# Performance work log

Hardware: AMD Instinct MI355X
Metric: run time of the kernel (lower is better)

Reference implementation:

```python
import jax, jax.numpy as jnp
import numpy as np

N = 500_000   # num nodes
F = 128       # num_features
H = 128       # hidden
B = 32_768    # batch size
K = 4         # hops
RWS = 16      # random walks per batch node
E = RWS * B   # sampled edges per hop
ALPHA = 0.1
OUT = 8


def setup_inputs() -> dict:
    key = jax.random.key(0)
    ks = jax.random.split(key, 12)
    x = jax.random.normal(ks[0], (N, F), dtype=jnp.float32)
    degree = jax.random.uniform(ks[1], (N,), dtype=jnp.float32, minval=1.0, maxval=64.0)
    batch = jax.random.randint(ks[2], (B,), 0, N, dtype=jnp.int32)
    heads_idx = jax.random.randint(ks[3], (K, E), 0, B, dtype=jnp.int32)
    ends = jax.random.randint(ks[4], (K, E), 0, N, dtype=jnp.int32)
    # MLP params (Kaiming-ish scaling)
    W0 = jax.random.normal(ks[5], (F, H), dtype=jnp.float32) / np.float32(np.sqrt(F))
    b0 = jnp.zeros((H,), dtype=jnp.float32)
    W1 = jax.random.normal(ks[6], (H, H), dtype=jnp.float32) / np.float32(np.sqrt(H))
    b1 = jnp.zeros((H,), dtype=jnp.float32)
    W2 = jax.random.normal(ks[7], (H, OUT), dtype=jnp.float32) / np.float32(np.sqrt(H))
    b2 = jnp.zeros((OUT,), dtype=jnp.float32)
    # APPNP attention weights: alpha*(1-alpha)^k, last = (1-alpha)^K
    att = np.float32(ALPHA) * np.float32(1.0 - ALPHA) ** np.arange(K + 1, dtype=np.float32)
    att[-1] = np.float32(1.0 - ALPHA) ** np.float32(K)
    att = jnp.asarray(att)
    return {"x": x, "W0": W0, "b0": b0, "W1": W1, "b1": b1, "W2": W2, "b2": b2,
            "att": att, "degree": degree, "batch": batch,
            "heads_idx": heads_idx, "ends": ends}


def reference(x, W0, b0, W1, b1, W2, b2, att, degree, batch, heads_idx, ends):
    # eval mode: dropout is a no-op
    dis = degree ** -0.5  # deg_inv_sqrt

    def mlp(feats):  # lins[1](relu(lins[0](feats)))
        h = jax.nn.relu(feats @ W0 + b0)
        return h @ W1 + b1

    nb = batch.shape[0]
    ne = jnp.float32(ends.shape[1])
    dsum = degree[batch].sum()

    aggx = att[0] * mlp(x[batch])                       # [B, H]
    for k in range(K):  # small fixed hop count
        heads = heads_idx[k]                            # local rows in [0, B)
        e = ends[k]                                     # global node ids
        val = dis[batch[heads]] * dis[e] * (dsum / ne)  # [E]
        tmp = mlp(x[e]) * val[:, None]                  # gather + MLP + weight
        aggx = aggx + att[k + 1] * jax.ops.segment_sum(tmp, heads, num_segments=nb)
    out = jax.nn.relu(aggx) @ W2 + b2                   # [B, 8]
    return jax.nn.log_softmax(out, axis=1)
```

## Files before the change

kernel.cpp:

```cpp
#include <hip/hip_runtime.h>

#define NN 500000
#define FF 128
#define HH 128
#define BB 32768
#define KHOPS 4
#define EPER 524288
#define KE (KHOPS * EPER)
#define NOUT 8
#define SBLK 512
#define EPB (KE / SBLK)

typedef unsigned short u16;
typedef unsigned char u8;
typedef __attribute__((ext_vector_type(8))) short short8v;
typedef __attribute__((ext_vector_type(4))) float f32x4;

__device__ __forceinline__ float bflo(unsigned int u) {
    union { unsigned int x; float f; } t; t.x = u << 16; return t.f;
}
__device__ __forceinline__ float bfhi(unsigned int u) {
    union { unsigned int x; float f; } t; t.x = u & 0xFFFF0000u; return t.f;
}
__device__ __forceinline__ u16 f2bf(float f) {
    union { float f; unsigned int u; } t; t.f = f;
    unsigned int u = t.u;
    unsigned int r = (u + 0x7FFFu + ((u >> 16) & 1u)) >> 16;
    return (u16)r;
}

__global__ void k_degsum1(const float* __restrict__ deg, const int* __restrict__ batch,
                          float* __restrict__ partial) {
    __shared__ float red[256];
    int i = blockIdx.x * 256 + threadIdx.x;
    red[threadIdx.x] = deg[batch[i]];
    __syncthreads();
    for (int off = 128; off > 0; off >>= 1) {
        if (threadIdx.x < off) red[threadIdx.x] += red[threadIdx.x + off];
        __syncthreads();
    }
    if (threadIdx.x == 0) partial[blockIdx.x] = red[0];
}
__global__ void k_degsum2(const float* __restrict__ partial, float* __restrict__ dsum) {
    __shared__ float red[128];
    red[threadIdx.x] = partial[threadIdx.x];
    __syncthreads();
    for (int off = 64; off > 0; off >>= 1) {
        if (threadIdx.x < off) red[threadIdx.x] += red[threadIdx.x + off];
        __syncthreads();
    }
    if (threadIdx.x == 0) *dsum = red[0];
}

__global__ void k_prep(const float* __restrict__ deg, const int* __restrict__ batch,
                       const float* __restrict__ dsum,
                       float* __restrict__ dis, float* __restrict__ disb) {
    int i = blockIdx.x * 256 + threadIdx.x;
    if (i < NN) dis[i] = rsqrtf(deg[i]);
    if (i < BB) disb[i] = rsqrtf(deg[batch[i]]) * (dsum[0] * (1.0f / (float)EPER));
}

__launch_bounds__(256, 2)
__global__ void k_hist2(const int* __restrict__ heads, u8* __restrict__ M) {
    __shared__ unsigned int hp[8192];
    int tid = threadIdx.x, blk = blockIdx.x;
    #pragma unroll
    for (int j = 0; j < 32; j++) hp[tid + j * 256] = 0;
    __syncthreads();
    int ebase = blk * EPB;
    #pragma unroll 4
    for (int it = 0; it < EPB / 256; it++) {
        int b = heads[ebase + it * 256 + tid];
        atomicAdd(&hp[b >> 2], 1u << ((b & 3) * 8));
    }
    __syncthreads();
    unsigned int* M32 = (unsigned int*)(M + (size_t)blk * BB);
    #pragma unroll
    for (int j = 0; j < 32; j++) {
        int w = tid + j * 256;
        M32[w] = hp[w];
    }
}

__global__ void k_colscan(u8* __restrict__ M, int* __restrict__ colsum) {
    int key = blockIdx.x * 256 + threadIdx.x;
    unsigned int run = 0;
    #pragma unroll 8
    for (int b = 0; b < SBLK; b++) {
        size_t idx = (size_t)b * BB + key;
        u8 v = M[idx];
        M[idx] = (u8)run;
        run += v;
    }
    colsum[key] = (int)run;
}

__global__ void k_scan(const int* __restrict__ colsum, int* __restrict__ base) {
    __shared__ int sc[1024];
    int tid = threadIdx.x;
    int loc[32];
    int run = 0;
    #pragma unroll
    for (int j = 0; j < 32; j++) {
        loc[j] = run;
        run += colsum[tid * 32 + j];
    }
    sc[tid] = run;
    __syncthreads();
    for (int off = 1; off < 1024; off <<= 1) {
        int v = (tid >= off) ? sc[tid - off] : 0;
        __syncthreads();
        sc[tid] += v;
        __syncthreads();
    }
    int excl = sc[tid] - run;
    #pragma unroll
    for (int j = 0; j < 32; j++) base[tid * 32 + j] = excl + loc[j];
    if (tid == 1023) base[BB] = sc[1023];
}

__launch_bounds__(256, 2)
__global__ void k_scatter2(const int* __restrict__ heads, const int* __restrict__ ends,
                           const u8* __restrict__ M, const int* __restrict__ base,
                           const float* __restrict__ dis, const float* __restrict__ disb,
                           const float* __restrict__ att, uint2* __restrict__ ewp) {
    __shared__ unsigned int hp[8192];
    int tid = threadIdx.x, blk = blockIdx.x;
    float attk = att[(blk >> 7) + 1];
    #pragma unroll
    for (int j = 0; j < 32; j++) hp[tid + j * 256] = 0;
    __syncthreads();
    int ebase = blk * EPB;
    for (int it = 0; it < EPB / 256; it++) {
        int i = ebase + it * 256 + tid;
        int b = heads[i];
        int e = ends[i];
        float w = attk * disb[b] * dis[e];
        unsigned int old = atomicAdd(&hp[b >> 2], 1u << ((b & 3) * 8));
        unsigned int rank = (old >> ((b & 3) * 8)) & 0xFFu;
        int pos = base[b] + (int)M[(size_t)blk * BB + b] + (int)rank;
        uint2 pw;
        pw.x = (unsigned int)e;
        pw.y = __float_as_uint(w);
        ewp[pos] = pw;
    }
}

__global__ void k_packW0(const float* __restrict__ W0, u16* __restrict__ w0p) {
    int f = blockIdx.x * 256 + threadIdx.x;
    int k = f >> 7, c = f & 127;
    int kt = k >> 5, i = k & 7, lh = (k >> 3) & 3;
    int lane = lh * 16 + (c & 15), n = c >> 4;
    w0p[(((kt * 8 + n) * 64 + lane) << 3) + i] = f2bf(W0[f]);
}

__launch_bounds__(256, 2)
__global__ void k_gemm1(const float* __restrict__ x, const u16* __restrict__ w0p,
                        const float* __restrict__ b0, u16* __restrict__ h) {
    __shared__ u16 xs[128 * 128];
    __shared__ u16 ws[128 * 128];
    int tid = threadIdx.x;
    int wid = tid >> 6;
    int lane = tid & 63;
    long rowbase = (long)blockIdx.x * 128;

    #pragma unroll
    for (int r = 0; r < 8; r++) {
        int f = tid + r * 256;
        *(float4*)&ws[f * 8] = *(const float4*)&w0p[f * 8];
    }
    #pragma unroll
    for (int r = 0; r < 16; r++) {
        int f = tid + r * 256;
        int row = f >> 5;
        int c4 = (f & 31) * 4;
        long grow = rowbase + row; if (grow >= NN) grow = NN - 1;
        float4 v = *(const float4*)&x[grow * 128 + c4];
        ushort4 pv;
        pv.x = f2bf(v.x); pv.y = f2bf(v.y); pv.z = f2bf(v.z); pv.w = f2bf(v.w);
        int byte = row * 256 + ((c4 * 2) ^ ((row & 7) << 4));
        *(ushort4*)((char*)xs + byte) = pv;
    }
    __syncthreads();

    short8v a[2][4];
    #pragma unroll
    for (int rs = 0; rs < 2; rs++) {
        int row = wid * 32 + rs * 16 + (lane & 15);
        int sw = (row & 7) << 4;
        #pragma unroll
        for (int kt = 0; kt < 4; kt++) {
            int kb = kt * 64 + (lane >> 4) * 16;
            a[rs][kt] = *(const short8v*)((const char*)xs + row * 256 + (kb ^ sw));
        }
    }

    f32x4 acc[2][8] = {};
    #pragma unroll
    for (int n = 0; n < 8; n++) {
        short8v bfr[4];
        #pragma unroll
        for (int kt = 0; kt < 4; kt++)
            bfr[kt] = *(const short8v*)&ws[(((kt * 8 + n) * 64 + lane) << 3)];
        #pragma unroll
        for (int rs = 0; rs < 2; rs++) {
            #pragma unroll
            for (int kt = 0; kt < 4; kt++)
                acc[rs][n] = __builtin_amdgcn_mfma_f32_16x16x32_bf16(
                                 a[rs][kt], bfr[kt], acc[rs][n], 0, 0, 0);
        }
    }

    float b0v[8];
    #pragma unroll
    for (int n = 0; n < 8; n++) b0v[n] = b0[n * 16 + (lane & 15)];
    #pragma unroll
    for (int rs = 0; rs < 2; rs++) {
        #pragma unroll
        for (int r = 0; r < 4; r++) {
            long grow = rowbase + wid * 32 + rs * 16 + (lane >> 4) * 4 + r;
            if (grow < NN) {
                #pragma unroll
                for (int n = 0; n < 8; n++) {
                    float v = acc[rs][n][r] + b0v[n];
                    v = v > 0.f ? v : 0.f;
                    h[grow * 128 + n * 16 + (lane & 15)] = f2bf(v);
                }
            }
        }
    }
}

__launch_bounds__(256)
__global__ void k_gather(const u16* __restrict__ h, const int* __restrict__ batch,
                         const int* __restrict__ base, const uint2* __restrict__ ewp,
                         const float* __restrict__ att,
                         float* __restrict__ P, float* __restrict__ s) {
    int b = blockIdx.x * 4 + (threadIdx.x >> 6);
    int l = threadIdx.x & 63;
    int q = l >> 4;
    int c8 = (l & 15) * 8;
    float att0 = att[0];
    float acc[8] = {0.f, 0.f, 0.f, 0.f, 0.f, 0.f, 0.f, 0.f};

    if (q == 0) {
        int nb = batch[b];
        uint4 v = *(const uint4*)&h[(size_t)nb * 128 + c8];
        acc[0] = att0 * bflo(v.x); acc[1] = att0 * bfhi(v.x);
        acc[2] = att0 * bflo(v.y); acc[3] = att0 * bfhi(v.y);
        acc[4] = att0 * bflo(v.z); acc[5] = att0 * bfhi(v.z);
        acc[6] = att0 * bflo(v.w); acc[7] = att0 * bfhi(v.w);
    }

    int beg = base[b], fin = base[b + 1];
    float wsum = 0.f;
    for (int j = beg; j < fin; j += 32) {
        uint2 pw[8];
        #pragma unroll
        for (int u = 0; u < 8; u++) {
            int je = j + u * 4 + q;
            int jc = je < fin ? je : beg;
            pw[u] = ewp[jc];
            if (je >= fin) pw[u].y = 0u;
        }
        uint4 v[8];
        #pragma unroll
        for (int u = 0; u < 8; u++)
            v[u] = *(const uint4*)&h[(size_t)pw[u].x * 128 + c8];
        #pragma unroll
        for (int u = 0; u < 8; u++) {
            float w = __uint_as_float(pw[u].y);
            acc[0] += w * bflo(v[u].x); acc[1] += w * bfhi(v[u].x);
            acc[2] += w * bflo(v[u].y); acc[3] += w * bfhi(v[u].y);
            acc[4] += w * bflo(v[u].z); acc[5] += w * bfhi(v[u].z);
            acc[6] += w * bflo(v[u].w); acc[7] += w * bfhi(v[u].w);
            wsum += w;
        }
    }
    #pragma unroll
    for (int k = 0; k < 8; k++) {
        acc[k] += __shfl_xor(acc[k], 16);
        acc[k] += __shfl_xor(acc[k], 32);
    }
    wsum += __shfl_xor(wsum, 16);
    wsum += __shfl_xor(wsum, 32);

    if (q == 0) {
        float4 o0 = { acc[0], acc[1], acc[2], acc[3] };
        float4 o1 = { acc[4], acc[5], acc[6], acc[7] };
        *(float4*)&P[(size_t)b * 128 + c8]     = o0;
        *(float4*)&P[(size_t)b * 128 + c8 + 4] = o1;
        if (l == 0) s[b] = att0 + wsum;
    }
}

__launch_bounds__(256, 2)
__global__ void k_out(const float* __restrict__ P, const float* __restrict__ s,
                      const float* __restrict__ W1, const float* __restrict__ b1,
                      const float* __restrict__ W2, const float* __restrict__ b2,
                      float* __restrict__ out) {
    __shared__ float W1s[128 * 128];
    __shared__ float Ps[32 * 128];
    int tid = threadIdx.x;
    int rowbase = blockIdx.x * 32;
    #pragma unroll
    for (int rep = 0; rep < 16; rep++) {
        int f = tid + rep * 256;
        *(float4*)&W1s[f * 4] = *(const float4*)&W1[f * 4];
    }
    #pragma unroll
    for (int rep = 0; rep < 4; rep++) {
        int f = tid + rep * 256;
        *(float4*)&Ps[f * 4] = *(const float4*)&P[(size_t)rowbase * 128 + f * 4];
    }
    __syncthreads();

    int c0 = (tid & 31) * 4;
    int r0 = (tid >> 5) * 4;
    float b1r[4] = { b1[c0], b1[c0 + 1], b1[c0 + 2], b1[c0 + 3] };
    float sv[4];
    #pragma unroll
    for (int j = 0; j < 4; j++) sv[j] = s[rowbase + r0 + j];

    float acc[4][4] = {};
    #pragma unroll 2
    for (int i = 0; i < 128; i += 4) {
        float4 xq[4], wq4[4];
        #pragma unroll
        for (int j = 0; j < 4; j++) xq[j]  = *(const float4*)&Ps[(r0 + j) * 128 + i];
        #pragma unroll
        for (int q = 0; q < 4; q++) wq4[q] = *(const float4*)&W1s[(i + q) * 128 + c0];
        #pragma unroll
        for (int j = 0; j < 4; j++) {
            float xv[4] = { xq[j].x, xq[j].y, xq[j].z, xq[j].w };
            #pragma unroll
            for (int q = 0; q < 4; q++) {
                acc[j][0] += xv[q] * wq4[q].x;
                acc[j][1] += xv[q] * wq4[q].y;
                acc[j][2] += xv[q] * wq4[q].z;
                acc[j][3] += xv[q] * wq4[q].w;
            }
        }
    }
    __syncthreads();
    #pragma unroll
    for (int j = 0; j < 4; j++) {
        #pragma unroll
        for (int c = 0; c < 4; c++) {
            float v = acc[j][c] + sv[j] * b1r[c];
            Ps[(r0 + j) * 128 + c0 + c] = v > 0.f ? v : 0.f;
        }
    }
    __syncthreads();

    int row = tid >> 3;
    int o = tid & 7;
    int rot = (row * 4) & 127;
    float v = b2[o];
    #pragma unroll 4
    for (int ii = 0; ii < 128; ii++) {
        int i = (ii + rot) & 127;
        v += Ps[row * 128 + i] * W2[i * 8 + o];
    }
    float m = v;
    for (int d = 1; d < 8; d <<= 1) m = fmaxf(m, __shfl_xor(m, d, 8));
    float ex = expf(v - m);
    float sum = ex;
    for (int d = 1; d < 8; d <<= 1) sum += __shfl_xor(sum, d, 8);
    out[(size_t)(rowbase + row) * 8 + o] = (v - m) - logf(sum);
}

extern "C" void kernel_launch(void* const* d_in, const int* in_sizes, int n_in,
                              void* d_out, int out_size, void* d_ws, size_t ws_size,
                              hipStream_t stream) {
    const float* x     = (const float*)d_in[0];
    const float* W0    = (const float*)d_in[1];
    const float* b0    = (const float*)d_in[2];
    const float* W1    = (const float*)d_in[3];
    const float* b1    = (const float*)d_in[4];
    const float* W2    = (const float*)d_in[5];
    const float* b2    = (const float*)d_in[6];
    const float* att   = (const float*)d_in[7];
    const float* deg   = (const float*)d_in[8];
    const int*   batch = (const int*)d_in[9];
    const int*   heads = (const int*)d_in[10];
    const int*   ends  = (const int*)d_in[11];
    float* out = (float*)d_out;

    char* w = (char*)d_ws;
    size_t off = 0;
    u16* h = (u16*)(w + off);          off += (size_t)NN * 128 * 2;
    float* P = (float*)(w + off);      off += (size_t)BB * 128 * 4;
    float* s = (float*)(w + off);      off += (size_t)BB * 4;
    int* base = (int*)(w + off);       off += 131328;
    uint2* ewp = (uint2*)(w + off);    off += (size_t)KE * 8;
    u8* M = (u8*)(w + off);            off += (size_t)SBLK * BB;
    int* colsum = (int*)(w + off);     off += (size_t)BB * 4;
    float* dis = (float*)(w + off);    off += (size_t)NN * 4;
    float* disb = (float*)(w + off);   off += (size_t)BB * 4;
    float* partial = (float*)(w + off); off += 1024;
    float* dsum = (float*)(w + off);   off += 256;
    u16* w0p = (u16*)(w + off);        off += 16384 * 2;

    k_degsum1<<<128, 256, 0, stream>>>(deg, batch, partial);
    k_degsum2<<<1, 128, 0, stream>>>(partial, dsum);
    k_prep<<<(NN + 255) / 256, 256, 0, stream>>>(deg, batch, dsum, dis, disb);
    k_hist2<<<SBLK, 256, 0, stream>>>(heads, M);
    k_colscan<<<BB / 256, 256, 0, stream>>>(M, colsum);
    k_scan<<<1, 1024, 0, stream>>>(colsum, base);
    k_scatter2<<<SBLK, 256, 0, stream>>>(heads, ends, M, base, dis, disb, att, ewp);
    k_packW0<<<64, 256, 0, stream>>>(W0, w0p);
    k_gemm1<<<(NN + 127) / 128, 256, 0, stream>>>(x, w0p, b0, h);
    k_gather<<<BB / 4, 256, 0, stream>>>(h, batch, base, ewp, att, P, s);
    k_out<<<BB / 32, 256, 0, stream>>>(P, s, W1, b1, W2, b2, out);
}
```

Before: 336.4 us.

## Pack edge entries to 32 bits, compute weights in gather, coalesce gemm1 stores

Edge records shrink from 8-byte (node, weight) pairs to a 4-byte word holding the node id and hop index. The gather kernel now recomputes the weight from dis, disb and att, which removes scattered work from the scatter kernel but adds a random dis[e] load per edge. The gemm1 epilogue stages bf16 results through swizzled LDS so each wave writes whole 16-byte chunks of h instead of 2-byte scattered stores. The scatter block count is also halved.

```diff
diff --git a/kernel.cpp b/kernel.cpp
--- a/kernel.cpp
+++ b/kernel.cpp
@@ -8,7 +8,7 @@
 #define EPER 524288
 #define KE (KHOPS * EPER)
 #define NOUT 8
-#define SBLK 512
+#define SBLK 256
 #define EPB (KE / SBLK)
 
 typedef unsigned short u16;
@@ -122,11 +122,9 @@
 __launch_bounds__(256, 2)
 __global__ void k_scatter2(const int* __restrict__ heads, const int* __restrict__ ends,
                            const u8* __restrict__ M, const int* __restrict__ base,
-                           const float* __restrict__ dis, const float* __restrict__ disb,
-                           const float* __restrict__ att, uint2* __restrict__ ewp) {
+                           unsigned int* __restrict__ pe) {
     __shared__ unsigned int hp[8192];
     int tid = threadIdx.x, blk = blockIdx.x;
-    float attk = att[(blk >> 7) + 1];
     #pragma unroll
     for (int j = 0; j < 32; j++) hp[tid + j * 256] = 0;
     __syncthreads();
@@ -134,15 +132,12 @@
     for (int it = 0; it < EPB / 256; it++) {
         int i = ebase + it * 256 + tid;
         int b = heads[i];
-        int e = ends[i];
-        float w = attk * disb[b] * dis[e];
+        unsigned int e = (unsigned int)ends[i];
+        unsigned int kk = (unsigned int)(i >> 19);
         unsigned int old = atomicAdd(&hp[b >> 2], 1u << ((b & 3) * 8));
         unsigned int rank = (old >> ((b & 3) * 8)) & 0xFFu;
         int pos = base[b] + (int)M[(size_t)blk * BB + b] + (int)rank;
-        uint2 pw;
-        pw.x = (unsigned int)e;
-        pw.y = __float_as_uint(w);
-        ewp[pos] = pw;
+        pe[pos] = (kk << 19) | e;
     }
 }
 
@@ -214,26 +209,41 @@
     float b0v[8];
     #pragma unroll
     for (int n = 0; n < 8; n++) b0v[n] = b0[n * 16 + (lane & 15)];
+
+    u16* xw = &xs[wid * 32 * 128];
     #pragma unroll
     for (int rs = 0; rs < 2; rs++) {
         #pragma unroll
         for (int r = 0; r < 4; r++) {
-            long grow = rowbase + wid * 32 + rs * 16 + (lane >> 4) * 4 + r;
-            if (grow < NN) {
-                #pragma unroll
-                for (int n = 0; n < 8; n++) {
-                    float v = acc[rs][n][r] + b0v[n];
-                    v = v > 0.f ? v : 0.f;
-                    h[grow * 128 + n * 16 + (lane & 15)] = f2bf(v);
-                }
+            int row = rs * 16 + (lane >> 4) * 4 + r;
+            int sw = (row & 7) << 4;
+            #pragma unroll
+            for (int n = 0; n < 8; n++) {
+                float v = acc[rs][n][r] + b0v[n];
+                v = v > 0.f ? v : 0.f;
+                int byte = row * 256 + ((n * 32 + (lane & 15) * 2) ^ sw);
+                *(u16*)((char*)xw + byte) = f2bf(v);
             }
         }
+    }
+    __syncthreads();
+    #pragma unroll
+    for (int pass = 0; pass < 8; pass++) {
+        int off = pass * 1024 + lane * 16;
+        int row = off >> 8;
+        int colb = off & 255;
+        int ocolb = colb ^ ((row & 7) << 4);
+        long grow = rowbase + wid * 32 + row;
+        uint4 v = *(const uint4*)((const char*)xw + off);
+        if (grow < NN)
+            *(uint4*)((char*)&h[grow * 128] + ocolb) = v;
     }
 }
 
 __launch_bounds__(256)
 __global__ void k_gather(const u16* __restrict__ h, const int* __restrict__ batch,
-                         const int* __restrict__ base, const uint2* __restrict__ ewp,
+                         const int* __restrict__ base, const unsigned int* __restrict__ pe,
+                         const float* __restrict__ dis, const float* __restrict__ disb,
                          const float* __restrict__ att,
                          float* __restrict__ P, float* __restrict__ s) {
     int b = blockIdx.x * 4 + (threadIdx.x >> 6);
@@ -241,6 +251,8 @@
     int q = l >> 4;
     int c8 = (l & 15) * 8;
     float att0 = att[0];
+    float a1 = att[1], a2 = att[2], a3 = att[3], a4 = att[4];
+    float dbv = disb[b];
     float acc[8] = {0.f, 0.f, 0.f, 0.f, 0.f, 0.f, 0.f, 0.f};
 
     if (q == 0) {
@@ -255,21 +267,28 @@
     int beg = base[b], fin = base[b + 1];
     float wsum = 0.f;
     for (int j = beg; j < fin; j += 32) {
-        uint2 pw[8];
+        unsigned int p[8];
         #pragma unroll
         for (int u = 0; u < 8; u++) {
             int je = j + u * 4 + q;
             int jc = je < fin ? je : beg;
-            pw[u] = ewp[jc];
-            if (je >= fin) pw[u].y = 0u;
-        }
+            p[u] = pe[jc];
+            if (je >= fin) p[u] |= 0x80000000u;
+        }
+        float wv[8];
         uint4 v[8];
         #pragma unroll
-        for (int u = 0; u < 8; u++)
-            v[u] = *(const uint4*)&h[(size_t)pw[u].x * 128 + c8];
-        #pragma unroll
         for (int u = 0; u < 8; u++) {
-            float w = __uint_as_float(pw[u].y);
+            int e = (int)(p[u] & 0x7FFFFu);
+            int kk = (int)((p[u] >> 19) & 3u);
+            float av = (kk < 2) ? (kk == 0 ? a1 : a2) : (kk == 2 ? a3 : a4);
+            float w = av * dbv * dis[e];
+            wv[u] = (p[u] & 0x80000000u) ? 0.f : w;
+            v[u] = *(const uint4*)&h[(size_t)e * 128 + c8];
+        }
+        #pragma unroll
+        for (int u = 0; u < 8; u++) {
+            float w = wv[u];
             acc[0] += w * bflo(v[u].x); acc[1] += w * bfhi(v[u].x);
             acc[2] += w * bflo(v[u].y); acc[3] += w * bfhi(v[u].y);
             acc[4] += w * bflo(v[u].z); acc[5] += w * bfhi(v[u].z);
@@ -393,7 +412,7 @@
     float* P = (float*)(w + off);      off += (size_t)BB * 128 * 4;
     float* s = (float*)(w + off);      off += (size_t)BB * 4;
     int* base = (int*)(w + off);       off += 131328;
-    uint2* ewp = (uint2*)(w + off);    off += (size_t)KE * 8;
+    unsigned int* pe = (unsigned int*)(w + off); off += (size_t)KE * 4;
     u8* M = (u8*)(w + off);            off += (size_t)SBLK * BB;
     int* colsum = (int*)(w + off);     off += (size_t)BB * 4;
     float* dis = (float*)(w + off);    off += (size_t)NN * 4;
@@ -408,9 +427,9 @@
     k_hist2<<<SBLK, 256, 0, stream>>>(heads, M);
     k_colscan<<<BB / 256, 256, 0, stream>>>(M, colsum);
     k_scan<<<1, 1024, 0, stream>>>(colsum, base);
-    k_scatter2<<<SBLK, 256, 0, stream>>>(heads, ends, M, base, dis, disb, att, ewp);
+    k_scatter2<<<SBLK, 256, 0, stream>>>(heads, ends, M, base, pe);
     k_packW0<<<64, 256, 0, stream>>>(W0, w0p);
     k_gemm1<<<(NN + 127) / 128, 256, 0, stream>>>(x, w0p, b0, h);
-    k_gather<<<BB / 4, 256, 0, stream>>>(h, batch, base, ewp, att, P, s);
+    k_gather<<<BB / 4, 256, 0, stream>>>(h, batch, base, pe, dis, disb, att, P, s);
     k_out<<<BB / 32, 256, 0, stream>>>(P, s, W1, b1, W2, b2, out);
 }
```

After: 313.7 us. 6.8% less time.

## Fuse preprocessing kernels, overlap edge scatter with GEMM, and coalesce hidden stores

Applied to the files above, without the earlier changes.

Merges the degree sum, dis computation, W0 packing and per-block histogram into one launch. Column scan and disb go into a second launch, and the column scan now works on packed 32-bit words. The edge scatter and the x·W0 GEMM share one launch so the latency-bound scatter blocks can run alongside the compute tiles. Scatter blocks are halved in number (SBLK 512→256), which shrinks the M matrix and the colscan work. GEMM outputs are staged through swizzled LDS so h is written with 16-byte coalesced stores, and the gather uses packed 2-wide FMAs. The packed byte prefix sums would carry into the next byte if any key's total count exceeded 255, and the GEMM blocks now declare 64 KB of LDS even when only the scatter path runs.

```diff
diff --git a/kernel.cpp b/kernel.cpp
--- a/kernel.cpp
+++ b/kernel.cpp
@@ -8,13 +8,15 @@
 #define EPER 524288
 #define KE (KHOPS * EPER)
 #define NOUT 8
-#define SBLK 512
+#define SBLK 256
 #define EPB (KE / SBLK)
+#define GEMM_TILES 3907
 
 typedef unsigned short u16;
 typedef unsigned char u8;
 typedef __attribute__((ext_vector_type(8))) short short8v;
 typedef __attribute__((ext_vector_type(4))) float f32x4;
+typedef __attribute__((ext_vector_type(2))) float f32x2;
 
 __device__ __forceinline__ float bflo(unsigned int u) {
     union { unsigned int x; float f; } t; t.x = u << 16; return t.f;
@@ -29,70 +31,95 @@
     return (u16)r;
 }
 
-__global__ void k_degsum1(const float* __restrict__ deg, const int* __restrict__ batch,
-                          float* __restrict__ partial) {
-    __shared__ float red[256];
-    int i = blockIdx.x * 256 + threadIdx.x;
-    red[threadIdx.x] = deg[batch[i]];
-    __syncthreads();
-    for (int off = 128; off > 0; off >>= 1) {
-        if (threadIdx.x < off) red[threadIdx.x] += red[threadIdx.x + off];
-        __syncthreads();
-    }
-    if (threadIdx.x == 0) partial[blockIdx.x] = red[0];
-}
-__global__ void k_degsum2(const float* __restrict__ partial, float* __restrict__ dsum) {
-    __shared__ float red[128];
-    red[threadIdx.x] = partial[threadIdx.x];
-    __syncthreads();
-    for (int off = 64; off > 0; off >>= 1) {
-        if (threadIdx.x < off) red[threadIdx.x] += red[threadIdx.x + off];
-        __syncthreads();
-    }
-    if (threadIdx.x == 0) *dsum = red[0];
-}
-
-__global__ void k_prep(const float* __restrict__ deg, const int* __restrict__ batch,
-                       const float* __restrict__ dsum,
-                       float* __restrict__ dis, float* __restrict__ disb) {
-    int i = blockIdx.x * 256 + threadIdx.x;
-    if (i < NN) dis[i] = rsqrtf(deg[i]);
-    if (i < BB) disb[i] = rsqrtf(deg[batch[i]]) * (dsum[0] * (1.0f / (float)EPER));
-}
-
 __launch_bounds__(256, 2)
-__global__ void k_hist2(const int* __restrict__ heads, u8* __restrict__ M) {
+__global__ void k_pre1(const int* __restrict__ heads, u8* __restrict__ M,
+                       const float* __restrict__ deg, const int* __restrict__ batch,
+                       float* __restrict__ dsum, const float* __restrict__ W0,
+                       u16* __restrict__ w0p, float* __restrict__ dis) {
     __shared__ unsigned int hp[8192];
-    int tid = threadIdx.x, blk = blockIdx.x;
-    #pragma unroll
-    for (int j = 0; j < 32; j++) hp[tid + j * 256] = 0;
-    __syncthreads();
-    int ebase = blk * EPB;
-    #pragma unroll 4
-    for (int it = 0; it < EPB / 256; it++) {
-        int b = heads[ebase + it * 256 + tid];
-        atomicAdd(&hp[b >> 2], 1u << ((b & 3) * 8));
-    }
-    __syncthreads();
-    unsigned int* M32 = (unsigned int*)(M + (size_t)blk * BB);
-    #pragma unroll
-    for (int j = 0; j < 32; j++) {
-        int w = tid + j * 256;
-        M32[w] = hp[w];
-    }
-}
-
-__global__ void k_colscan(u8* __restrict__ M, int* __restrict__ colsum) {
-    int key = blockIdx.x * 256 + threadIdx.x;
-    unsigned int run = 0;
-    #pragma unroll 8
-    for (int b = 0; b < SBLK; b++) {
-        size_t idx = (size_t)b * BB + key;
-        u8 v = M[idx];
-        M[idx] = (u8)run;
-        run += v;
-    }
-    colsum[key] = (int)run;
+    int tid = threadIdx.x;
+    int bid = blockIdx.x;
+    if (bid < SBLK) {
+        #pragma unroll
+        for (int j = 0; j < 32; j++) hp[tid + j * 256] = 0;
+        __syncthreads();
+        int ebase = bid * EPB;
+        #pragma unroll 4
+        for (int it = 0; it < EPB / 256; it++) {
+            int b = heads[ebase + it * 256 + tid];
+            atomicAdd(&hp[b >> 2], 1u << ((b & 3) * 8));
+        }
+        __syncthreads();
+        unsigned int* M32 = (unsigned int*)(M + (size_t)bid * BB);
+        #pragma unroll
+        for (int j = 0; j < 32; j++) {
+            int w = tid + j * 256;
+            M32[w] = hp[w];
+        }
+    } else if (bid == SBLK) {
+        float* red = (float*)hp;
+        float a0 = 0.f, a1 = 0.f, a2 = 0.f, a3 = 0.f;
+        for (int i = tid; i < BB; i += 1024) {
+            a0 += deg[batch[i]];
+            a1 += deg[batch[i + 256]];
+            a2 += deg[batch[i + 512]];
+            a3 += deg[batch[i + 768]];
+        }
+        red[tid] = (a0 + a1) + (a2 + a3);
+        __syncthreads();
+        for (int off = 128; off > 0; off >>= 1) {
+            if (tid < off) red[tid] += red[tid + off];
+            __syncthreads();
+        }
+        if (tid == 0) dsum[0] = red[0];
+    } else if (bid == SBLK + 1) {
+        for (int r = 0; r < 64; r++) {
+            int f = r * 256 + tid;
+            int k = f >> 7, c = f & 127;
+            int kt = k >> 5, i = k & 7, lh = (k >> 3) & 3;
+            int lane = lh * 16 + (c & 15), n = c >> 4;
+            w0p[(((kt * 8 + n) * 64 + lane) << 3) + i] = f2bf(W0[f]);
+        }
+    } else {
+        int i0 = (bid - SBLK - 2) * 1024 + tid * 4;
+        if (i0 < NN) {
+            float4 d = *(const float4*)&deg[i0];
+            float4 o;
+            o.x = rsqrtf(d.x); o.y = rsqrtf(d.y);
+            o.z = rsqrtf(d.z); o.w = rsqrtf(d.w);
+            *(float4*)&dis[i0] = o;
+        }
+    }
+}
+
+__global__ void k_pre2(u8* __restrict__ M, int* __restrict__ colsum,
+                       const float* __restrict__ deg, const int* __restrict__ batch,
+                       const float* __restrict__ dsum, float* __restrict__ disb) {
+    int tid = threadIdx.x;
+    if (blockIdx.x < 32) {
+        int g = blockIdx.x * 256 + tid;
+        unsigned int* M32 = (unsigned int*)M;
+        unsigned int run = 0;
+        #pragma unroll 8
+        for (int b = 0; b < SBLK; b++) {
+            size_t idx = (size_t)b * (BB / 4) + g;
+            unsigned int v = M32[idx];
+            M32[idx] = run;
+            run += v;
+        }
+        colsum[g * 4 + 0] = (int)(run & 0xFFu);
+        colsum[g * 4 + 1] = (int)((run >> 8) & 0xFFu);
+        colsum[g * 4 + 2] = (int)((run >> 16) & 0xFFu);
+        colsum[g * 4 + 3] = (int)((run >> 24) & 0xFFu);
+    } else {
+        int b0 = (blockIdx.x - 32) * 1024 + tid * 4;
+        float sc = dsum[0] * (1.0f / (float)EPER);
+        #pragma unroll
+        for (int t = 0; t < 4; t++) {
+            int b = b0 + t;
+            disb[b] = rsqrtf(deg[batch[b]]) * sc;
+        }
+    }
 }
 
 __global__ void k_scan(const int* __restrict__ colsum, int* __restrict__ base) {
@@ -120,49 +147,44 @@
 }
 
 __launch_bounds__(256, 2)
-__global__ void k_scatter2(const int* __restrict__ heads, const int* __restrict__ ends,
-                           const u8* __restrict__ M, const int* __restrict__ base,
-                           const float* __restrict__ dis, const float* __restrict__ disb,
-                           const float* __restrict__ att, uint2* __restrict__ ewp) {
-    __shared__ unsigned int hp[8192];
-    int tid = threadIdx.x, blk = blockIdx.x;
-    float attk = att[(blk >> 7) + 1];
-    #pragma unroll
-    for (int j = 0; j < 32; j++) hp[tid + j * 256] = 0;
-    __syncthreads();
-    int ebase = blk * EPB;
-    for (int it = 0; it < EPB / 256; it++) {
-        int i = ebase + it * 256 + tid;
-        int b = heads[i];
-        int e = ends[i];
-        float w = attk * disb[b] * dis[e];
-        unsigned int old = atomicAdd(&hp[b >> 2], 1u << ((b & 3) * 8));
-        unsigned int rank = (old >> ((b & 3) * 8)) & 0xFFu;
-        int pos = base[b] + (int)M[(size_t)blk * BB + b] + (int)rank;
-        uint2 pw;
-        pw.x = (unsigned int)e;
-        pw.y = __float_as_uint(w);
-        ewp[pos] = pw;
-    }
-}
-
-__global__ void k_packW0(const float* __restrict__ W0, u16* __restrict__ w0p) {
-    int f = blockIdx.x * 256 + threadIdx.x;
-    int k = f >> 7, c = f & 127;
-    int kt = k >> 5, i = k & 7, lh = (k >> 3) & 3;
-    int lane = lh * 16 + (c & 15), n = c >> 4;
-    w0p[(((kt * 8 + n) * 64 + lane) << 3) + i] = f2bf(W0[f]);
-}
-
-__launch_bounds__(256, 2)
-__global__ void k_gemm1(const float* __restrict__ x, const u16* __restrict__ w0p,
-                        const float* __restrict__ b0, u16* __restrict__ h) {
-    __shared__ u16 xs[128 * 128];
-    __shared__ u16 ws[128 * 128];
+__global__ void k_fused(const float* __restrict__ x, const u16* __restrict__ w0p,
+                        const float* __restrict__ b0, u16* __restrict__ h,
+                        const int* __restrict__ heads, const int* __restrict__ ends,
+                        const u8* __restrict__ M, const int* __restrict__ base,
+                        const float* __restrict__ dis, const float* __restrict__ disb,
+                        const float* __restrict__ att, uint2* __restrict__ ewp) {
+    __shared__ char smem[65536];
     int tid = threadIdx.x;
+
+    if (blockIdx.x < SBLK) {
+        unsigned int* hp = (unsigned int*)smem;
+        int blk = blockIdx.x;
+        float attk = att[(blk >> 6) + 1];
+        #pragma unroll
+        for (int j = 0; j < 32; j++) hp[tid + j * 256] = 0;
+        __syncthreads();
+        int ebase = blk * EPB;
+        for (int it = 0; it < EPB / 256; it++) {
+            int i = ebase + it * 256 + tid;
+            int b = heads[i];
+            int e = ends[i];
+            float w = attk * disb[b] * dis[e];
+            unsigned int old = atomicAdd(&hp[b >> 2], 1u << ((b & 3) * 8));
+            unsigned int rank = (old >> ((b & 3) * 8)) & 0xFFu;
+            int pos = base[b] + (int)M[(size_t)blk * BB + b] + (int)rank;
+            uint2 pw;
+            pw.x = (unsigned int)e;
+            pw.y = __float_as_uint(w);
+            ewp[pos] = pw;
+        }
+        return;
+    }
+
+    u16* xs = (u16*)smem;
+    u16* ws = (u16*)(smem + 32768);
     int wid = tid >> 6;
     int lane = tid & 63;
-    long rowbase = (long)blockIdx.x * 128;
+    long rowbase = (long)(blockIdx.x - SBLK) * 128;
 
     #pragma unroll
     for (int r = 0; r < 8; r++) {
@@ -214,20 +236,34 @@
     float b0v[8];
     #pragma unroll
     for (int n = 0; n < 8; n++) b0v[n] = b0[n * 16 + (lane & 15)];
+
+    u16* xw = &xs[wid * 32 * 128];
     #pragma unroll
     for (int rs = 0; rs < 2; rs++) {
         #pragma unroll
         for (int r = 0; r < 4; r++) {
-            long grow = rowbase + wid * 32 + rs * 16 + (lane >> 4) * 4 + r;
-            if (grow < NN) {
-                #pragma unroll
-                for (int n = 0; n < 8; n++) {
-                    float v = acc[rs][n][r] + b0v[n];
-                    v = v > 0.f ? v : 0.f;
-                    h[grow * 128 + n * 16 + (lane & 15)] = f2bf(v);
-                }
+            int row = rs * 16 + (lane >> 4) * 4 + r;
+            int sw = (row & 7) << 4;
+            #pragma unroll
+            for (int n = 0; n < 8; n++) {
+                float v = acc[rs][n][r] + b0v[n];
+                v = v > 0.f ? v : 0.f;
+                int byte = row * 256 + ((n * 32 + (lane & 15) * 2) ^ sw);
+                *(u16*)((char*)xw + byte) = f2bf(v);
             }
         }
+    }
+    __syncthreads();
+    #pragma unroll
+    for (int pass = 0; pass < 8; pass++) {
+        int off = pass * 1024 + lane * 16;
+        int row = off >> 8;
+        int colb = off & 255;
+        int ocolb = colb ^ ((row & 7) << 4);
+        long grow = rowbase + wid * 32 + row;
+        uint4 v = *(const uint4*)((const char*)xw + off);
+        if (grow < NN)
+            *(uint4*)((char*)&h[grow * 128] + ocolb) = v;
     }
 }
 
@@ -241,19 +277,19 @@
     int q = l >> 4;
     int c8 = (l & 15) * 8;
     float att0 = att[0];
-    float acc[8] = {0.f, 0.f, 0.f, 0.f, 0.f, 0.f, 0.f, 0.f};
+    f32x2 acc2[4] = {{0.f, 0.f}, {0.f, 0.f}, {0.f, 0.f}, {0.f, 0.f}};
+    float wsum = 0.f;
 
     if (q == 0) {
         int nb = batch[b];
         uint4 v = *(const uint4*)&h[(size_t)nb * 128 + c8];
-        acc[0] = att0 * bflo(v.x); acc[1] = att0 * bfhi(v.x);
-        acc[2] = att0 * bflo(v.y); acc[3] = att0 * bfhi(v.y);
-        acc[4] = att0 * bflo(v.z); acc[5] = att0 * bfhi(v.z);
-        acc[6] = att0 * bflo(v.w); acc[7] = att0 * bfhi(v.w);
+        acc2[0] = f32x2{att0 * bflo(v.x), att0 * bfhi(v.x)};
+        acc2[1] = f32x2{att0 * bflo(v.y), att0 * bfhi(v.y)};
+        acc2[2] = f32x2{att0 * bflo(v.z), att0 * bfhi(v.z)};
+        acc2[3] = f32x2{att0 * bflo(v.w), att0 * bfhi(v.w)};
     }
 
     int beg = base[b], fin = base[b + 1];
-    float wsum = 0.f;
     for (int j = beg; j < fin; j += 32) {
         uint2 pw[8];
         #pragma unroll
@@ -270,24 +306,27 @@
         #pragma unroll
         for (int u = 0; u < 8; u++) {
             float w = __uint_as_float(pw[u].y);
-            acc[0] += w * bflo(v[u].x); acc[1] += w * bfhi(v[u].x);
-            acc[2] += w * bflo(v[u].y); acc[3] += w * bfhi(v[u].y);
-            acc[4] += w * bflo(v[u].z); acc[5] += w * bfhi(v[u].z);
-            acc[6] += w * bflo(v[u].w); acc[7] += w * bfhi(v[u].w);
+            f32x2 w2 = {w, w};
+            acc2[0] = __builtin_elementwise_fma(w2, f32x2{bflo(v[u].x), bfhi(v[u].x)}, acc2[0]);
+            acc2[1] = __builtin_elementwise_fma(w2, f32x2{bflo(v[u].y), bfhi(v[u].y)}, acc2[1]);
+            acc2[2] = __builtin_elementwise_fma(w2, f32x2{bflo(v[u].z), bfhi(v[u].z)}, acc2[2]);
+            acc2[3] = __builtin_elementwise_fma(w2, f32x2{bflo(v[u].w), bfhi(v[u].w)}, acc2[3]);
             wsum += w;
         }
     }
+    float accf[8] = { acc2[0].x, acc2[0].y, acc2[1].x, acc2[1].y,
+                      acc2[2].x, acc2[2].y, acc2[3].x, acc2[3].y };
     #pragma unroll
     for (int k = 0; k < 8; k++) {
-        acc[k] += __shfl_xor(acc[k], 16);
-        acc[k] += __shfl_xor(acc[k], 32);
+        accf[k] += __shfl_xor(accf[k], 16);
+        accf[k] += __shfl_xor(accf[k], 32);
     }
     wsum += __shfl_xor(wsum, 16);
     wsum += __shfl_xor(wsum, 32);
 
     if (q == 0) {
-        float4 o0 = { acc[0], acc[1], acc[2], acc[3] };
-        float4 o1 = { acc[4], acc[5], acc[6], acc[7] };
+        float4 o0 = { accf[0], accf[1], accf[2], accf[3] };
+        float4 o1 = { accf[4], accf[5], accf[6], accf[7] };
         *(float4*)&P[(size_t)b * 128 + c8]     = o0;
         *(float4*)&P[(size_t)b * 128 + c8 + 4] = o1;
         if (l == 0) s[b] = att0 + wsum;
@@ -398,19 +437,16 @@
     int* colsum = (int*)(w + off);     off += (size_t)BB * 4;
     float* dis = (float*)(w + off);    off += (size_t)NN * 4;
     float* disb = (float*)(w + off);   off += (size_t)BB * 4;
-    float* partial = (float*)(w + off); off += 1024;
     float* dsum = (float*)(w + off);   off += 256;
     u16* w0p = (u16*)(w + off);        off += 16384 * 2;
 
-    k_degsum1<<<128, 256, 0, stream>>>(deg, batch, partial);
-    k_degsum2<<<1, 128, 0, stream>>>(partial, dsum);
-    k_prep<<<(NN + 255) / 256, 256, 0, stream>>>(deg, batch, dsum, dis, disb);
-    k_hist2<<<SBLK, 256, 0, stream>>>(heads, M);
-    k_colscan<<<BB / 256, 256, 0, stream>>>(M, colsum);
+    int disBlocks = (NN + 1023) / 1024;
+    k_pre1<<<SBLK + 2 + disBlocks, 256, 0, stream>>>(heads, M, deg, batch,
+                                                     dsum, W0, w0p, dis);
+    k_pre2<<<64, 256, 0, stream>>>(M, colsum, deg, batch, dsum, disb);
     k_scan<<<1, 1024, 0, stream>>>(colsum, base);
-    k_scatter2<<<SBLK, 256, 0, stream>>>(heads, ends, M, base, dis, disb, att, ewp);
-    k_packW0<<<64, 256, 0, stream>>>(W0, w0p);
-    k_gemm1<<<(NN + 127) / 128, 256, 0, stream>>>(x, w0p, b0, h);
+    k_fused<<<SBLK + GEMM_TILES, 256, 0, stream>>>(x, w0p, b0, h, heads, ends,
+                                                   M, base, dis, disb, att, ewp);
     k_gather<<<BB / 4, 256, 0, stream>>>(h, batch, base, ewp, att, P, s);
     k_out<<<BB / 32, 256, 0, stream>>>(P, s, W1, b1, W2, b2, out);
 }
```

Result: slower. 347.9 us (+3.4%).
